# Kernel optimization log

Measured on AMD Instinct MI355X. Metric: run time of the kernel, lower is better.

## Reference

```python
import jax, jax.numpy as jnp
import numpy as np

N, K, CONV_DIM = 100, 20, 256
TEMP, ALPHA = 0.1, 0.1
B_NORM = 1  # module hardcodes self.B = 1
BATCH = 8


def setup_inputs() -> dict:
    key = jax.random.key(0)
    inputs = jax.random.normal(key, (BATCH, N, K, CONV_DIM), dtype=jnp.float32)
    return {"inputs": inputs}


def reference(inputs) -> jnp.ndarray:
    # inputs: [B, N, K, D] prototype representations
    B, n, k, D = inputs.shape
    # L2-normalize along feature dim (reduce_euclidean_norm)
    xn = inputs / jnp.sqrt(jnp.sum(inputs * inputs, axis=-1, keepdims=True))
    flat = xn.reshape(B, n * k, D)  # all prototypes, all classes: [B, N*K, D]

    # anchor-vs-all similarities: [B, N, K, N*K]
    sims = jnp.einsum('bnkd,bmd->bnkm', xn, flat) / TEMP
    # anchor self-similarity (==1/t after normalization, but keep exact math): [B, N, K]
    self_sim = jnp.sum(xn * xn, axis=-1) / TEMP

    # denominator: sum_m exp(sim) - exp(self)
    denom = jnp.sum(jnp.exp(sims), axis=-1) - jnp.exp(self_sim)
    log_term = jnp.log(denom)  # [B, N, K]

    # intra-class similarity sum: anchor vs all K prototypes of its own class
    intra = jnp.einsum('bnkd,bnjd->bnk', xn, xn) / TEMP  # [B, N, K]
    sum_term = (intra - self_sim) / (k - 1)

    cl_loss = jnp.sum(log_term - sum_term)  # summed over batch and all N*K anchors
    loss = ALPHA * cl_loss / (B_NORM * n * k * D)
    return loss
```

## Files before the change

### kernel.cpp

```cpp
#include <hip/hip_runtime.h>
#include <math.h>

#define BB 8
#define NN 100
#define KK 20
#define DD 256
#define MM 2000
#define MP 2048
#define NTILE 136
#define GRID2 (BB * NTILE)
#define TINV 10.0f
#define LOSS_SCALE 1.953125e-7f

typedef __bf16 bf16x8 __attribute__((ext_vector_type(8)));
typedef float floatx4 __attribute__((ext_vector_type(4)));
typedef __attribute__((address_space(1))) const ushort GUshort;
typedef __attribute__((address_space(3))) ushort LUshort;

__device__ __forceinline__ ushort f2bf(float f) {
    unsigned int u = __float_as_uint(f);
    u += 0x7fffu + ((u >> 16) & 1u);
    return (ushort)(u >> 16);
}

__global__ void norm_bf16(const float* __restrict__ x, ushort* __restrict__ xb,
                          float* __restrict__ accbuf, unsigned int* __restrict__ ctr,
                          float* __restrict__ out) {
    if (blockIdx.x < 32)
        ((float4*)accbuf)[blockIdx.x * 256 + threadIdx.x] = make_float4(0.f, 0.f, 0.f, 0.f);
    if (blockIdx.x == 0 && threadIdx.x < BB) ctr[threadIdx.x] = 0u;
    if (blockIdx.x == 0 && threadIdx.x == 0) out[0] = 0.0f;

    const int rg = blockIdx.x * 4 + (threadIdx.x >> 6);
    const int lane = threadIdx.x & 63;
    const int b = rg >> 11;
    const int r = rg & (MP - 1);
    ushort4 outv = make_ushort4(0, 0, 0, 0);
    if (r < MM) {
        const float4 v = ((const float4*)(x + ((size_t)(b * MM + r)) * DD))[lane];
        float s = v.x * v.x + v.y * v.y + v.z * v.z + v.w * v.w;
        #pragma unroll
        for (int o = 32; o >= 1; o >>= 1) s += __shfl_xor(s, o, 64);
        const float inv = 1.0f / sqrtf(s);
        outv.x = f2bf(v.x * inv);
        outv.y = f2bf(v.y * inv);
        outv.z = f2bf(v.z * inv);
        outv.w = f2bf(v.w * inv);
    }
    ((ushort4*)(xb + (size_t)rg * DD))[lane] = outv;
}

__global__ __launch_bounds__(256)
void cl_mfma(const ushort* __restrict__ xb,
             float* __restrict__ denom_g, float* __restrict__ intra_g,
             unsigned int* __restrict__ ctr, float* __restrict__ out) {
    __shared__ __align__(16) ushort As[128 * 64];
    __shared__ __align__(16) ushort Bs[128 * 64];

    const int b = blockIdx.x & 7;
    int rem = blockIdx.x >> 3;
    int ti = 0;
    while (rem >= 16 - ti) { rem -= 16 - ti; ++ti; }
    const int tj = ti + rem;
    const int rbase = ti << 7;
    const int cbase = tj << 7;
    const bool offdiag = (ti != tj);
    const ushort* __restrict__ xbb = xb + (size_t)b * MP * DD;

    const int tid = threadIdx.x;
    const int lane = tid & 63;
    const int w = tid >> 6;
    const int wr = (w >> 1) << 6;
    const int wc = (w & 1) << 6;
    const int tx = lane & 15;
    const int tx7 = tx & 7;
    const int quad = lane >> 4;

    const int srow = lane >> 3;
    const int sg = (lane & 7) ^ srow;

    floatx4 acc[4][4];
    #pragma unroll
    for (int mt = 0; mt < 4; ++mt)
        #pragma unroll
        for (int nt = 0; nt < 4; ++nt)
            acc[mt][nt] = (floatx4){0.f, 0.f, 0.f, 0.f};

    #pragma unroll 1
    for (int kc = 0; kc < 4; ++kc) {
        __syncthreads();
        #pragma unroll
        for (int q = 0; q < 4; ++q) {
            const int R = ((w << 2) + q) << 3;
            const size_t koff = (kc << 6) + (sg << 3);
            __builtin_amdgcn_global_load_lds(
                (GUshort*)(xbb + (size_t)(rbase + R + srow) * DD + koff),
                (LUshort*)(As + R * 64), 16, 0, 0);
            __builtin_amdgcn_global_load_lds(
                (GUshort*)(xbb + (size_t)(cbase + R + srow) * DD + koff),
                (LUshort*)(Bs + R * 64), 16, 0, 0);
        }
        __syncthreads();

        #pragma unroll
        for (int ks = 0; ks < 2; ++ks) {
            const int g = (ks << 2) + quad;
            const int gp = (g ^ tx7) << 3;
            bf16x8 af[4], bf[4];
            #pragma unroll
            for (int mt = 0; mt < 4; ++mt)
                af[mt] = *(const bf16x8*)(As + (wr + (mt << 4) + tx) * 64 + gp);
            #pragma unroll
            for (int nt = 0; nt < 4; ++nt)
                bf[nt] = *(const bf16x8*)(Bs + (wc + (nt << 4) + tx) * 64 + gp);
            #pragma unroll
            for (int mt = 0; mt < 4; ++mt)
                #pragma unroll
                for (int nt = 0; nt < 4; ++nt)
                    acc[mt][nt] = __builtin_amdgcn_mfma_f32_16x16x32_bf16(af[mt], bf[nt], acc[mt][nt], 0, 0, 0);
        }
    }

    int colv[4], colcls[4];
    bool colok[4];
    #pragma unroll
    for (int nt = 0; nt < 4; ++nt) {
        const int c = cbase + wc + (nt << 4) + tx;
        colv[nt] = c;
        colok[nt] = c < MM;
        colcls[nt] = c / KK;
    }
    float de_c[4] = {0.f, 0.f, 0.f, 0.f};
    float it_c[4] = {0.f, 0.f, 0.f, 0.f};

    #pragma unroll
    for (int mt = 0; mt < 4; ++mt) {
        #pragma unroll
        for (int i = 0; i < 4; ++i) {
            const int row = rbase + wr + (mt << 4) + (quad << 2) + i;
            const int rcls = row / KK;
            float de = 0.f, it = 0.f;
            #pragma unroll
            for (int nt = 0; nt < 4; ++nt) {
                const float sim = acc[mt][nt][i] * TINV;
                const bool ok = colok[nt] && (colv[nt] != row);
                const float e = ok ? __expf(sim) : 0.0f;
                const float sv = (ok && (colcls[nt] == rcls)) ? sim : 0.0f;
                de += e;
                it += sv;
                de_c[nt] += e;
                it_c[nt] += sv;
            }
            #pragma unroll
            for (int o = 8; o >= 1; o >>= 1) {
                de += __shfl_xor(de, o, 64);
                it += __shfl_xor(it, o, 64);
            }
            if (tx == 0) {
                atomicAdd(&denom_g[b * MP + row], de);
                atomicAdd(&intra_g[b * MP + row], it);
            }
        }
    }

    if (offdiag) {
        #pragma unroll
        for (int nt = 0; nt < 4; ++nt) {
            de_c[nt] += __shfl_xor(de_c[nt], 16, 64);
            de_c[nt] += __shfl_xor(de_c[nt], 32, 64);
            it_c[nt] += __shfl_xor(it_c[nt], 16, 64);
            it_c[nt] += __shfl_xor(it_c[nt], 32, 64);
        }
        if (quad == 0) {
            #pragma unroll
            for (int nt = 0; nt < 4; ++nt) {
                if (colok[nt]) {
                    atomicAdd(&denom_g[b * MP + colv[nt]], de_c[nt]);
                    atomicAdd(&intra_g[b * MP + colv[nt]], it_c[nt]);
                }
            }
        }
    }

    __syncthreads();
    unsigned int* tick = (unsigned int*)As;
    if (tid == 0) tick[0] = atomicAdd(&ctr[b], 1u);
    __syncthreads();
    if (tick[0] == NTILE - 1) {
        const float* dg = denom_g + b * MP;
        const float* ig = intra_g + b * MP;
        float dv[8], iv[8];
        #pragma unroll
        for (int k = 0; k < 8; ++k) {
            const int r2 = tid + (k << 8);
            const int rc = (r2 < MM) ? r2 : 0;
            dv[k] = __hip_atomic_load(&dg[rc], __ATOMIC_RELAXED, __HIP_MEMORY_SCOPE_AGENT);
            iv[k] = __hip_atomic_load(&ig[rc], __ATOMIC_RELAXED, __HIP_MEMORY_SCOPE_AGENT);
        }
        float s = 0.0f;
        #pragma unroll
        for (int k = 0; k < 8; ++k) {
            const int r2 = tid + (k << 8);
            const float t = logf(dv[k]) - iv[k] * (1.0f / (KK - 1));
            s += (r2 < MM) ? t : 0.0f;
        }
        #pragma unroll
        for (int o = 32; o >= 1; o >>= 1) s += __shfl_xor(s, o, 64);
        float* red = (float*)(As + 128);
        if (lane == 0) red[w] = s;
        __syncthreads();
        if (tid == 0)
            atomicAdd(out, (red[0] + red[1] + red[2] + red[3]) * LOSS_SCALE);
    }
}

extern "C" void kernel_launch(void* const* d_in, const int* in_sizes, int n_in,
                              void* d_out, int out_size, void* d_ws, size_t ws_size,
                              hipStream_t stream) {
    const float* x = (const float*)d_in[0];
    float* out = (float*)d_out;
    float* denom_g = (float*)d_ws;
    float* intra_g = denom_g + BB * MP;
    ushort* xb = (ushort*)(intra_g + BB * MP);
    unsigned int* ctr = (unsigned int*)(xb + (size_t)BB * MP * DD);

    norm_bf16<<<BB * MP / 4, 256, 0, stream>>>(x, xb, denom_g, ctr, out);
    cl_mfma<<<GRID2, 256, 0, stream>>>(xb, denom_g, intra_g, ctr, out);
}
```

Measured before the change: 105.7 us.

## Replace global float atomics with per-slice partial stores and final slice reduction

Each tile block now writes its row and column partial sums with plain agent-scope stores into one of 32 distinct slices per row, instead of using atomicAdd on a shared accumulator. The slice index is chosen so every (slice, batch, row) entry is written exactly once, which also removes the need to zero the accumulators in the normalization kernel. The last block per batch then sums all 32 slices per row before the log and loss reduction. Per-batch counters are spaced 16 apart to avoid sharing a cache line. This trades atomic contention for a larger workspace and a heavier serial final reduction in the last block.

```diff
diff --git a/kernel.cpp b/kernel.cpp
--- a/kernel.cpp
+++ b/kernel.cpp
@@ -9,6 +9,7 @@
 #define MP 2048
 #define NTILE 136
 #define GRID2 (BB * NTILE)
+#define NSLICE 32
 #define TINV 10.0f
 #define LOSS_SCALE 1.953125e-7f
 
@@ -23,12 +24,16 @@
     return (ushort)(u >> 16);
 }
 
+__device__ __forceinline__ void agent_store(float* p, float v) {
+    __hip_atomic_store(p, v, __ATOMIC_RELAXED, __HIP_MEMORY_SCOPE_AGENT);
+}
+__device__ __forceinline__ float agent_load(const float* p) {
+    return __hip_atomic_load(p, __ATOMIC_RELAXED, __HIP_MEMORY_SCOPE_AGENT);
+}
+
 __global__ void norm_bf16(const float* __restrict__ x, ushort* __restrict__ xb,
-                          float* __restrict__ accbuf, unsigned int* __restrict__ ctr,
-                          float* __restrict__ out) {
-    if (blockIdx.x < 32)
-        ((float4*)accbuf)[blockIdx.x * 256 + threadIdx.x] = make_float4(0.f, 0.f, 0.f, 0.f);
-    if (blockIdx.x == 0 && threadIdx.x < BB) ctr[threadIdx.x] = 0u;
+                          unsigned int* __restrict__ ctr, float* __restrict__ out) {
+    if (blockIdx.x == 0 && threadIdx.x < BB) ctr[threadIdx.x * 16] = 0u;
     if (blockIdx.x == 0 && threadIdx.x == 0) out[0] = 0.0f;
 
     const int rg = blockIdx.x * 4 + (threadIdx.x >> 6);
@@ -52,7 +57,7 @@
 
 __global__ __launch_bounds__(256)
 void cl_mfma(const ushort* __restrict__ xb,
-             float* __restrict__ denom_g, float* __restrict__ intra_g,
+             float* __restrict__ deS, float* __restrict__ itS,
              unsigned int* __restrict__ ctr, float* __restrict__ out) {
     __shared__ __align__(16) ushort As[128 * 64];
     __shared__ __align__(16) ushort Bs[128 * 64];
@@ -133,6 +138,11 @@
     float de_c[4] = {0.f, 0.f, 0.f, 0.f};
     float it_c[4] = {0.f, 0.f, 0.f, 0.f};
 
+    float* __restrict__ deR = deS + ((size_t)(((tj << 1) | (w & 1)) * BB + b)) * MP;
+    float* __restrict__ itR = itS + ((size_t)(((tj << 1) | (w & 1)) * BB + b)) * MP;
+    float* __restrict__ deC = deS + ((size_t)(((ti << 1) | (w >> 1)) * BB + b)) * MP;
+    float* __restrict__ itC = itS + ((size_t)(((ti << 1) | (w >> 1)) * BB + b)) * MP;
+
     #pragma unroll
     for (int mt = 0; mt < 4; ++mt) {
         #pragma unroll
@@ -157,8 +167,8 @@
                 it += __shfl_xor(it, o, 64);
             }
             if (tx == 0) {
-                atomicAdd(&denom_g[b * MP + row], de);
-                atomicAdd(&intra_g[b * MP + row], it);
+                agent_store(&deR[row], de);
+                agent_store(&itR[row], it);
             }
         }
     }
@@ -174,34 +184,28 @@
         if (quad == 0) {
             #pragma unroll
             for (int nt = 0; nt < 4; ++nt) {
-                if (colok[nt]) {
-                    atomicAdd(&denom_g[b * MP + colv[nt]], de_c[nt]);
-                    atomicAdd(&intra_g[b * MP + colv[nt]], it_c[nt]);
-                }
+                agent_store(&deC[colv[nt]], de_c[nt]);
+                agent_store(&itC[colv[nt]], it_c[nt]);
             }
         }
     }
 
     __syncthreads();
     unsigned int* tick = (unsigned int*)As;
-    if (tid == 0) tick[0] = atomicAdd(&ctr[b], 1u);
+    if (tid == 0) tick[0] = atomicAdd(&ctr[b * 16], 1u);
     __syncthreads();
     if (tick[0] == NTILE - 1) {
-        const float* dg = denom_g + b * MP;
-        const float* ig = intra_g + b * MP;
-        float dv[8], iv[8];
-        #pragma unroll
+        float s = 0.0f;
+        #pragma unroll 1
         for (int k = 0; k < 8; ++k) {
             const int r2 = tid + (k << 8);
-            const int rc = (r2 < MM) ? r2 : 0;
-            dv[k] = __hip_atomic_load(&dg[rc], __ATOMIC_RELAXED, __HIP_MEMORY_SCOPE_AGENT);
-            iv[k] = __hip_atomic_load(&ig[rc], __ATOMIC_RELAXED, __HIP_MEMORY_SCOPE_AGENT);
-        }
-        float s = 0.0f;
-        #pragma unroll
-        for (int k = 0; k < 8; ++k) {
-            const int r2 = tid + (k << 8);
-            const float t = logf(dv[k]) - iv[k] * (1.0f / (KK - 1));
+            float dsum = 0.0f, isum = 0.0f;
+            #pragma unroll
+            for (int sl = 0; sl < NSLICE; ++sl) {
+                dsum += agent_load(deS + ((size_t)(sl * BB + b)) * MP + r2);
+                isum += agent_load(itS + ((size_t)(sl * BB + b)) * MP + r2);
+            }
+            const float t = logf(dsum) - isum * (1.0f / (KK - 1));
             s += (r2 < MM) ? t : 0.0f;
         }
         #pragma unroll
@@ -219,11 +223,11 @@
                               hipStream_t stream) {
     const float* x = (const float*)d_in[0];
     float* out = (float*)d_out;
-    float* denom_g = (float*)d_ws;
-    float* intra_g = denom_g + BB * MP;
-    ushort* xb = (ushort*)(intra_g + BB * MP);
+    float* deS = (float*)d_ws;
+    float* itS = deS + NSLICE * BB * MP;
+    ushort* xb = (ushort*)(itS + NSLICE * BB * MP);
     unsigned int* ctr = (unsigned int*)(xb + (size_t)BB * MP * DD);
 
-    norm_bf16<<<BB * MP / 4, 256, 0, stream>>>(x, xb, denom_g, ctr, out);
-    cl_mfma<<<GRID2, 256, 0, stream>>>(xb, denom_g, intra_g, ctr, out);
-}
+    norm_bf16<<<BB * MP / 4, 256, 0, stream>>>(x, xb, ctr, out);
+    cl_mfma<<<GRID2, 256, 0, stream>>>(xb, deS, itS, ctr, out);
+}
```

Result: faster. 103.5 us (-2.1%).
